# Performance work log

Measured on AMD Instinct MI355X. Metric: run time of the kernel, lower is better.

The kernel has to match this reference:

```python
import jax, jax.numpy as jnp
import numpy as np

NUM_HEAD = 16
MASKED_BIAS = -10000.0


def setup_inputs() -> dict:
    key = jax.random.key(0)
    k1, k2, k3 = jax.random.split(key, 3)
    B, M, N = 2, 2048, 1024
    x = jax.random.normal(k1, (B, M, N), dtype=jnp.float32)
    w_attn = jax.random.normal(k2, (N, 3 * N), dtype=jnp.float32) * 0.02
    w_proj = jax.random.normal(k3, (N, N), dtype=jnp.float32) * 0.02
    b_attn = jnp.zeros((3 * N,), dtype=jnp.float32)
    b_proj = jnp.zeros((N,), dtype=jnp.float32)
    return {"x": x, "w_attn": w_attn, "w_proj": w_proj,
            "b_attn": b_attn, "b_proj": b_proj}


def reference(x, w_attn, w_proj, b_attn, b_proj):
    B, M, N = x.shape
    H = NUM_HEAD
    d = N // H  # head dim
    # fused QKV projection: [B,M,3N]
    qkv = jnp.einsum('bmn,nd->bmd', x, w_attn) + b_attn
    q, k, v = jnp.split(qkv, 3, axis=-1)
    # split heads -> [B,H,M,d]
    q = q.reshape(B, M, H, d).transpose(0, 2, 1, 3)
    k = k.reshape(B, M, H, d).transpose(0, 2, 1, 3)
    v = v.reshape(B, M, H, d).transpose(0, 2, 1, 3)
    # scaled dot-product scores [B,H,M,M]
    scores = jnp.einsum('bhqd,bhkd->bhqk', q, k) / jnp.sqrt(jnp.float32(d))
    causal = jnp.tril(jnp.ones((M, M), dtype=bool))  # GPT-2 bias buffer
    scores = jnp.where(causal, scores, jnp.float32(MASKED_BIAS))
    attn = jax.nn.softmax(scores, axis=-1)
    # context [B,H,M,d] -> [B,M,N]
    ctx = jnp.einsum('bhqk,bhkd->bhqd', attn, v)
    ctx = ctx.transpose(0, 2, 1, 3).reshape(B, M, N)
    # output projection
    out = jnp.einsum('bmn,no->bmo', ctx, w_proj) + b_proj
    return out
```

## Files before the change

### kernel.cpp

```cpp
#include <hip/hip_runtime.h>

typedef __attribute__((ext_vector_type(8))) __bf16 bf16x8;
typedef __attribute__((ext_vector_type(4))) __bf16 bf16x4;
typedef __attribute__((ext_vector_type(4))) float f32x4;
typedef __attribute__((ext_vector_type(4))) short short4v;

__device__ __forceinline__ void async_copy16(const void* g, void* l) {
    __builtin_amdgcn_global_load_lds(
        (const __attribute__((address_space(1))) void*)g,
        (__attribute__((address_space(3))) void*)l, 16, 0, 0);
}

__global__ __launch_bounds__(256) void prep_k(
    const float* __restrict__ x, __bf16* __restrict__ xb,
    const float* __restrict__ wa, __bf16* __restrict__ wAt,
    const float* __restrict__ wp, __bf16* __restrict__ wPt)
{
    __shared__ float tile[32][33];
    const int bx = blockIdx.x;
    if (bx < 2048) {
        size_t i = ((size_t)bx * 256 + threadIdx.x) * 8;
        float4 a = *(const float4*)&x[i];
        float4 b = *(const float4*)&x[i + 4];
        bf16x8 o;
        o[0] = (__bf16)a.x; o[1] = (__bf16)a.y; o[2] = (__bf16)a.z; o[3] = (__bf16)a.w;
        o[4] = (__bf16)b.x; o[5] = (__bf16)b.y; o[6] = (__bf16)b.z; o[7] = (__bf16)b.w;
        *(bf16x8*)&xb[i] = o;
        return;
    }
    const float* src; __bf16* dst; int R, C, c0, r0;
    if (bx < 5120) {
        int id = bx - 2048;
        src = wa; dst = wAt; R = 1024; C = 3072;
        c0 = (id % 96) * 32; r0 = (id / 96) * 32;
    } else {
        int id = bx - 5120;
        src = wp; dst = wPt; R = 1024; C = 1024;
        c0 = (id & 31) * 32; r0 = (id >> 5) * 32;
    }
    int tx = threadIdx.x & 31, ty = threadIdx.x >> 5;
    for (int i = ty; i < 32; i += 8)
        tile[i][tx] = src[(size_t)(r0 + i) * C + (c0 + tx)];
    __syncthreads();
    for (int i = ty; i < 32; i += 8)
        dst[(size_t)(c0 + i) * R + (r0 + tx)] = (__bf16)tile[tx][i];
}

template <int MODE, int TN>
__global__ __launch_bounds__(256) void gemm_bt(
    const __bf16* __restrict__ A, const __bf16* __restrict__ Bt,
    const float* __restrict__ bias, int K,
    __bf16* __restrict__ O0, __bf16* __restrict__ O1, __bf16* __restrict__ O2,
    float* __restrict__ Of)
{
    constexpr int NJ = TN / 32;
    __shared__ __align__(16) __bf16 lds_a[2][128 * 32];
    __shared__ __align__(16) __bf16 lds_b[2][TN * 32];
    const int row0 = blockIdx.x * 128;
    const int col0 = blockIdx.y * TN;
    const int tid  = threadIdx.x;
    const int lane = tid & 63;
    const int w    = tid >> 6;
    const int wm   = (w >> 1) * 64, wn = (w & 1) * (TN / 2);
    const int quad = lane >> 4, l16 = lane & 15;

    auto stage = [&](int pb, int kb) {
#pragma unroll
        for (int t = 0; t < 2; ++t) {
            int s = t * 256 + tid;
            int L = s >> 3, c = (s & 7) ^ (L & 7);
            int row = 2 * L + (c >> 2), ch = c & 3;
            async_copy16(&A[(size_t)(row0 + row) * K + kb + ch * 8],
                         (char*)&lds_a[pb][0] + (t * 256 + w * 64) * 16);
        }
#pragma unroll
        for (int t = 0; t < TN / 64; ++t) {
            int s = t * 256 + tid;
            int L = s >> 3, c = (s & 7) ^ (L & 7);
            int row = 2 * L + (c >> 2), ch = c & 3;
            async_copy16(&Bt[(size_t)(col0 + row) * K + kb + ch * 8],
                         (char*)&lds_b[pb][0] + (t * 256 + w * 64) * 16);
        }
    };

    const int nIter = K >> 5;
    f32x4 acc[4][NJ] = {};
    stage(0, 0);
    for (int it = 0; it < nIter; ++it) {
        __syncthreads();
        if (it + 1 < nIter) stage((it + 1) & 1, (it + 1) << 5);
        const __bf16* la = &lds_a[it & 1][0];
        const __bf16* lb = &lds_b[it & 1][0];
        bf16x8 af[4], bfr[NJ];
#pragma unroll
        for (int i = 0; i < 4; ++i) {
            int r = wm + i * 16 + l16;
            int L = r >> 1, g = ((r & 1) * 4 + quad) ^ (L & 7);
            af[i] = *(const bf16x8*)&la[L * 64 + g * 8];
        }
#pragma unroll
        for (int j = 0; j < NJ; ++j) {
            int r = wn + j * 16 + l16;
            int L = r >> 1, g = ((r & 1) * 4 + quad) ^ (L & 7);
            bfr[j] = *(const bf16x8*)&lb[L * 64 + g * 8];
        }
#pragma unroll
        for (int i = 0; i < 4; ++i)
#pragma unroll
            for (int j = 0; j < NJ; ++j)
                acc[i][j] = __builtin_amdgcn_mfma_f32_16x16x32_bf16(
                    af[i], bfr[j], acc[i][j], 0, 0, 0);
    }

#pragma unroll
    for (int i = 0; i < 4; ++i) {
        int grow = row0 + wm + i * 16 + quad * 4;
#pragma unroll
        for (int j = 0; j < NJ; ++j) {
            int gcol = col0 + wn + j * 16 + l16;
            float bv = bias[gcol];
            if constexpr (MODE == 0) {
                int which = gcol >> 10;
                int n  = gcol & 1023;
                int hh = n >> 6, dd = n & 63;
                int bb = grow >> 11, mm0 = grow & 2047;
                int bhh = bb * 16 + hh;
                if (which == 2) {
                    int w64 = mm0 & 63;
                    int mi = (mm0 & ~63) | (w64 & 32) | ((w64 & 12) << 1)
                             | ((w64 & 16) >> 2);
                    bf16x4 pk;
#pragma unroll
                    for (int r = 0; r < 4; ++r)
                        pk[r] = (__bf16)(acc[i][j][r] + bv);
                    *(bf16x4*)&O2[((size_t)bhh * 64 + dd) * 2048 + mi] = pk;
                } else {
#pragma unroll
                    for (int r = 0; r < 4; ++r) {
                        float v = acc[i][j][r] + bv;
                        if (which == 0)
                            O0[((size_t)bhh * 2048 + mm0 + r) * 64 + dd] =
                                (__bf16)(v * 0.18033688011112042f);
                        else
                            O1[((size_t)bhh * 2048 + mm0 + r) * 64 + dd] =
                                (__bf16)v;
                    }
                }
            } else {
#pragma unroll
                for (int r = 0; r < 4; ++r) {
                    int gr = grow + r;
                    Of[(size_t)gr * 1024 + gcol] = acc[i][j][r] + bv;
                }
            }
        }
    }
}

__global__ __launch_bounds__(256) void attn_kernel(
    const __bf16* __restrict__ Qh, const __bf16* __restrict__ Kh,
    const __bf16* __restrict__ Vt, __bf16* __restrict__ ctx)
{
    const int M = 2048, D = 64;
    const int bh = blockIdx.x;
    const int qt = 31 - blockIdx.y;
    const int b = bh >> 4, h = bh & 15;
    const int tid = threadIdx.x, lane = tid & 63, w = tid >> 6;
    const int quad = lane >> 4, l16 = lane & 15;

    const int q0 = qt * 64;
    const int nIter = qt + 1;

    __shared__ __align__(16) __bf16 lds_k[2][64 * 64];
    __shared__ __align__(16) __bf16 lds_v[2][64 * 64];

    const __bf16* Qp = Qh + (size_t)bh * M * D;
    const __bf16* Kp = Kh + (size_t)bh * M * D;
    const __bf16* Vp = Vt + (size_t)bh * D * M;

    const int qw = q0 + w * 16;

    bf16x8 qf[2];
#pragma unroll
    for (int c = 0; c < 2; ++c)
        qf[c] = *(const bf16x8*)
            &Qp[(size_t)(qw + l16) * D + c * 32 + quad * 8];

    f32x4 acc2[4] = {};
    f32x4 acc_s = {};
    const short4v ones2 = {0x3F80, 0x3F80, 0x3F80, 0x3F80};

    auto stage = [&](int pb, int kb) {
#pragma unroll
        for (int t = 0; t < 2; ++t) {
            int c = w * 128 + t * 64 + lane;
            int row = c >> 3, ch = c & 7;
            int gch = ch ^ (row & 7);
            async_copy16(&Kp[(size_t)(kb + row) * 64 + gch * 8],
                         (char*)&lds_k[pb][0] + (w * 128 + t * 64) * 16);
            async_copy16(&Vp[(size_t)row * M + kb + gch * 8],
                         (char*)&lds_v[pb][0] + (w * 128 + t * 64) * 16);
        }
    };

    stage(0, 0);

    for (int it = 0; it < nIter; ++it) {
        const int kb = it << 6;
        __syncthreads();
        if (it + 1 < nIter) stage((it + 1) & 1, kb + 64);
        const __bf16* kt = &lds_k[it & 1][0];
        const __bf16* vt = &lds_v[it & 1][0];

        f32x4 s[4];
#pragma unroll
        for (int t = 0; t < 4; ++t) {
            f32x4 tt = {};
#pragma unroll
            for (int c = 0; c < 2; ++c) {
                int ch = ((c << 2) + quad) ^ (l16 & 7);
                bf16x8 kf = *(const bf16x8*)
                    &kt[(((t << 4) + l16) << 6) + (ch << 3)];
                tt = __builtin_amdgcn_mfma_f32_16x16x32_bf16(
                    kf, qf[c], tt, 0, 0, 0);
            }
            s[t] = tt;
        }
        if (kb + 63 > qw) {
#pragma unroll
            for (int t = 0; t < 4; ++t)
#pragma unroll
                for (int r = 0; r < 4; ++r)
                    if (kb + t * 16 + quad * 4 + r > qw + l16)
                        s[t][r] = -1e30f;
        }
        short4v pf[4];
#pragma unroll
        for (int t = 0; t < 4; ++t) {
            bf16x4 pk;
#pragma unroll
            for (int r = 0; r < 4; ++r)
                pk[r] = (__bf16)exp2f(s[t][r]);
            pf[t] = *(short4v*)&pk;
        }
#pragma unroll
        for (int f = 0; f < 4; ++f) {
            int row = (f << 4) + l16;
#pragma unroll
            for (int tp = 0; tp < 2; ++tp) {
                int g = ((tp << 2) + quad) ^ (row & 7);
                bf16x8 vv = *(const bf16x8*)&vt[(row << 6) + (g << 3)];
                bf16x4 lo = {vv[0], vv[1], vv[2], vv[3]};
                bf16x4 hi = {vv[4], vv[5], vv[6], vv[7]};
                acc2[f] = __builtin_amdgcn_mfma_f32_16x16x16bf16_1k(
                    *(short4v*)&lo, pf[2 * tp], acc2[f], 0, 0, 0);
                acc2[f] = __builtin_amdgcn_mfma_f32_16x16x16bf16_1k(
                    *(short4v*)&hi, pf[2 * tp + 1], acc2[f], 0, 0, 0);
            }
        }
#pragma unroll
        for (int t = 0; t < 4; ++t)
            acc_s = __builtin_amdgcn_mfma_f32_16x16x16bf16_1k(
                ones2, pf[t], acc_s, 0, 0, 0);
    }

    __syncthreads();
    __bf16* ldsT = &lds_k[0][0];
    const float l = acc_s[0];
#pragma unroll
    for (int f = 0; f < 4; ++f) {
        bf16x4 ov;
#pragma unroll
        for (int r = 0; r < 4; ++r)
            ov[r] = (__bf16)(acc2[f][r] / l);
        *(bf16x4*)&ldsT[(w * 16 + l16) * 72 + f * 16 + quad * 4] = ov;
    }
    __syncthreads();
    {
        int qq = tid >> 2;
        int dp = (tid & 3) * 16;
        const __bf16* src = &ldsT[qq * 72 + dp];
        __bf16* dst = &ctx[((size_t)(b * 2048 + q0 + qq)) * 1024 + h * 64 + dp];
        *(bf16x8*)&dst[0] = *(const bf16x8*)&src[0];
        *(bf16x8*)&dst[8] = *(const bf16x8*)&src[8];
    }
}

extern "C" void kernel_launch(void* const* d_in, const int* in_sizes, int n_in,
                              void* d_out, int out_size, void* d_ws, size_t ws_size,
                              hipStream_t stream) {
    const float* x      = (const float*)d_in[0];
    const float* w_attn = (const float*)d_in[1];
    const float* w_proj = (const float*)d_in[2];
    const float* b_attn = (const float*)d_in[3];
    const float* b_proj = (const float*)d_in[4];
    float* out = (float*)d_out;

    char* ws = (char*)d_ws;
    __bf16* xb  = (__bf16*)(ws);
    __bf16* ctx = (__bf16*)(ws);
    __bf16* wAt = (__bf16*)(ws + 8388608);
    __bf16* wPt = (__bf16*)(ws + 14680064);
    __bf16* Vt  = (__bf16*)(ws + 16777216);
    __bf16* Qh  = (__bf16*)d_out;
    __bf16* Kh  = (__bf16*)d_out + 4194304;

    prep_k<<<6144, 256, 0, stream>>>(x, xb, w_attn, wAt, w_proj, wPt);
    gemm_bt<0, 128><<<dim3(32, 24), 256, 0, stream>>>(xb, wAt, b_attn, 1024,
                                                      Qh, Kh, Vt, nullptr);
    attn_kernel<<<dim3(32, 32), 256, 0, stream>>>(Qh, Kh, Vt, ctx);
    gemm_bt<1, 64><<<dim3(32, 16), 256, 0, stream>>>(ctx, wPt, b_proj, 1024,
                                                     nullptr, nullptr, nullptr, out);
}
```

Baseline: 177.6 us.

## Split long causal attention tiles across two blocks and combine partial sums

The 16 longest query tiles per head are each split into two key-range halves run by separate blocks. Each half writes an unnormalized numerator and its row sums, and a new combine kernel adds the halves and normalizes. The goal is to even out the triangular causal workload and shorten the tail of the attention grid. The change also adds an early skip for fully masked key blocks per wave and replaces pairs of 16x16x16 MFMAs with single 16x16x32 MFMAs. Costs are an extra kernel launch, extra global traffic for the partials, and an extra bf16 rounding of the unnormalized partial numerators.

```diff
diff --git a/kernel.cpp b/kernel.cpp
--- a/kernel.cpp
+++ b/kernel.cpp
@@ -3,7 +3,6 @@
 typedef __attribute__((ext_vector_type(8))) __bf16 bf16x8;
 typedef __attribute__((ext_vector_type(4))) __bf16 bf16x4;
 typedef __attribute__((ext_vector_type(4))) float f32x4;
-typedef __attribute__((ext_vector_type(4))) short short4v;
 
 __device__ __forceinline__ void async_copy16(const void* g, void* l) {
     __builtin_amdgcn_global_load_lds(
@@ -159,17 +158,29 @@
 
 __global__ __launch_bounds__(256) void attn_kernel(
     const __bf16* __restrict__ Qh, const __bf16* __restrict__ Kh,
-    const __bf16* __restrict__ Vt, __bf16* __restrict__ ctx)
+    const __bf16* __restrict__ Vt, __bf16* __restrict__ ctx,
+    __bf16* __restrict__ pnum, float* __restrict__ lbuf)
 {
     const int M = 2048, D = 64;
     const int bh = blockIdx.x;
-    const int qt = 31 - blockIdx.y;
+    const int y = blockIdx.y;
     const int b = bh >> 4, h = bh & 15;
     const int tid = threadIdx.x, lane = tid & 63, w = tid >> 6;
     const int quad = lane >> 4, l16 = lane & 15;
 
+    int qt, part, t0, t1;
+    bool split;
+    if (y < 32) {
+        qt = 31 - (y >> 1); part = y & 1; split = true;
+        int half = (qt + 1) >> 1;
+        t0 = part ? half : 0;
+        t1 = part ? (qt + 1) : half;
+    } else {
+        qt = 47 - y; part = 0; split = false;
+        t0 = 0; t1 = qt + 1;
+    }
     const int q0 = qt * 64;
-    const int nIter = qt + 1;
+    const int nIter = t1 - t0;
 
     __shared__ __align__(16) __bf16 lds_k[2][64 * 64];
     __shared__ __align__(16) __bf16 lds_v[2][64 * 64];
@@ -188,7 +199,8 @@
 
     f32x4 acc2[4] = {};
     f32x4 acc_s = {};
-    const short4v ones2 = {0x3F80, 0x3F80, 0x3F80, 0x3F80};
+    const __bf16 onev = (__bf16)1.0f;
+    const bf16x8 ones8 = {onev, onev, onev, onev, onev, onev, onev, onev};
 
     auto stage = [&](int pb, int kb) {
 #pragma unroll
@@ -203,14 +215,15 @@
         }
     };
 
-    stage(0, 0);
-
-    for (int it = 0; it < nIter; ++it) {
-        const int kb = it << 6;
+    stage(0, t0 << 6);
+
+    for (int i = 0; i < nIter; ++i) {
+        const int kb = (t0 + i) << 6;
         __syncthreads();
-        if (it + 1 < nIter) stage((it + 1) & 1, kb + 64);
-        const __bf16* kt = &lds_k[it & 1][0];
-        const __bf16* vt = &lds_v[it & 1][0];
+        if (i + 1 < nIter) stage((i + 1) & 1, kb + 64);
+        if (kb > qw + 15) continue;
+        const __bf16* kt = &lds_k[i & 1][0];
+        const __bf16* vt = &lds_v[i & 1][0];
 
         f32x4 s[4];
 #pragma unroll
@@ -234,14 +247,16 @@
                     if (kb + t * 16 + quad * 4 + r > qw + l16)
                         s[t][r] = -1e30f;
         }
-        short4v pf[4];
-#pragma unroll
-        for (int t = 0; t < 4; ++t) {
-            bf16x4 pk;
-#pragma unroll
-            for (int r = 0; r < 4; ++r)
-                pk[r] = (__bf16)exp2f(s[t][r]);
-            pf[t] = *(short4v*)&pk;
+        bf16x8 pf32[2];
+#pragma unroll
+        for (int tp = 0; tp < 2; ++tp) {
+            bf16x8 pp;
+#pragma unroll
+            for (int r = 0; r < 4; ++r) {
+                pp[r]     = (__bf16)exp2f(s[2 * tp][r]);
+                pp[4 + r] = (__bf16)exp2f(s[2 * tp + 1][r]);
+            }
+            pf32[tp] = pp;
         }
 #pragma unroll
         for (int f = 0; f < 4; ++f) {
@@ -250,29 +265,30 @@
             for (int tp = 0; tp < 2; ++tp) {
                 int g = ((tp << 2) + quad) ^ (row & 7);
                 bf16x8 vv = *(const bf16x8*)&vt[(row << 6) + (g << 3)];
-                bf16x4 lo = {vv[0], vv[1], vv[2], vv[3]};
-                bf16x4 hi = {vv[4], vv[5], vv[6], vv[7]};
-                acc2[f] = __builtin_amdgcn_mfma_f32_16x16x16bf16_1k(
-                    *(short4v*)&lo, pf[2 * tp], acc2[f], 0, 0, 0);
-                acc2[f] = __builtin_amdgcn_mfma_f32_16x16x16bf16_1k(
-                    *(short4v*)&hi, pf[2 * tp + 1], acc2[f], 0, 0, 0);
+                acc2[f] = __builtin_amdgcn_mfma_f32_16x16x32_bf16(
+                    vv, pf32[tp], acc2[f], 0, 0, 0);
             }
         }
 #pragma unroll
-        for (int t = 0; t < 4; ++t)
-            acc_s = __builtin_amdgcn_mfma_f32_16x16x16bf16_1k(
-                ones2, pf[t], acc_s, 0, 0, 0);
+        for (int tp = 0; tp < 2; ++tp)
+            acc_s = __builtin_amdgcn_mfma_f32_16x16x32_bf16(
+                ones8, pf32[tp], acc_s, 0, 0, 0);
     }
 
     __syncthreads();
     __bf16* ldsT = &lds_k[0][0];
     const float l = acc_s[0];
+    const int tileIdx = bh * 16 + (qt - 16);
+    if (split && quad == 0)
+        lbuf[tileIdx * 128 + part * 64 + w * 16 + l16] = l;
 #pragma unroll
     for (int f = 0; f < 4; ++f) {
         bf16x4 ov;
 #pragma unroll
-        for (int r = 0; r < 4; ++r)
-            ov[r] = (__bf16)(acc2[f][r] / l);
+        for (int r = 0; r < 4; ++r) {
+            float v = acc2[f][r];
+            ov[r] = (__bf16)(split ? v : v / l);
+        }
         *(bf16x4*)&ldsT[(w * 16 + l16) * 72 + f * 16 + quad * 4] = ov;
     }
     __syncthreads();
@@ -280,10 +296,43 @@
         int qq = tid >> 2;
         int dp = (tid & 3) * 16;
         const __bf16* src = &ldsT[qq * 72 + dp];
-        __bf16* dst = &ctx[((size_t)(b * 2048 + q0 + qq)) * 1024 + h * 64 + dp];
+        __bf16* dst;
+        if (split && part == 1)
+            dst = &pnum[(size_t)tileIdx * 4096 + qq * 64 + dp];
+        else
+            dst = &ctx[((size_t)(b * 2048 + q0 + qq)) * 1024 + h * 64 + dp];
         *(bf16x8*)&dst[0] = *(const bf16x8*)&src[0];
         *(bf16x8*)&dst[8] = *(const bf16x8*)&src[8];
     }
+}
+
+__global__ __launch_bounds__(256) void combine_k(
+    __bf16* __restrict__ ctx, const __bf16* __restrict__ pnum,
+    const float* __restrict__ lbuf)
+{
+    const int bh = blockIdx.x, t = blockIdx.y;
+    const int b = bh >> 4, h = bh & 15;
+    const int tileIdx = bh * 16 + t;
+    const int q0 = (16 + t) * 64;
+    const int tid = threadIdx.x;
+    const int qq = tid >> 2, dp = (tid & 3) * 16;
+
+    float la = lbuf[tileIdx * 128 + qq];
+    float lb = lbuf[tileIdx * 128 + 64 + qq];
+    float inv = 1.0f / (la + lb);
+
+    __bf16* crow = &ctx[((size_t)(b * 2048 + q0 + qq)) * 1024 + h * 64 + dp];
+    const __bf16* prow = &pnum[(size_t)tileIdx * 4096 + qq * 64 + dp];
+    bf16x8 a0 = *(const bf16x8*)&crow[0], a1 = *(const bf16x8*)&crow[8];
+    bf16x8 b0 = *(const bf16x8*)&prow[0], b1 = *(const bf16x8*)&prow[8];
+    bf16x8 o0, o1;
+#pragma unroll
+    for (int e = 0; e < 8; ++e) {
+        o0[e] = (__bf16)(((float)a0[e] + (float)b0[e]) * inv);
+        o1[e] = (__bf16)(((float)a1[e] + (float)b1[e]) * inv);
+    }
+    *(bf16x8*)&crow[0] = o0;
+    *(bf16x8*)&crow[8] = o1;
 }
 
 extern "C" void kernel_launch(void* const* d_in, const int* in_sizes, int n_in,
@@ -297,18 +346,21 @@
     float* out = (float*)d_out;
 
     char* ws = (char*)d_ws;
-    __bf16* xb  = (__bf16*)(ws);
-    __bf16* ctx = (__bf16*)(ws);
-    __bf16* wAt = (__bf16*)(ws + 8388608);
-    __bf16* wPt = (__bf16*)(ws + 14680064);
-    __bf16* Vt  = (__bf16*)(ws + 16777216);
-    __bf16* Qh  = (__bf16*)d_out;
-    __bf16* Kh  = (__bf16*)d_out + 4194304;
+    __bf16* xb   = (__bf16*)(ws);
+    __bf16* ctx  = (__bf16*)(ws);
+    __bf16* wAt  = (__bf16*)(ws + 8388608);
+    __bf16* pnum = (__bf16*)(ws + 8388608);
+    float*  lbuf = (float*)(ws + 12582912);
+    __bf16* wPt  = (__bf16*)(ws + 14680064);
+    __bf16* Vt   = (__bf16*)(ws + 16777216);
+    __bf16* Qh   = (__bf16*)d_out;
+    __bf16* Kh   = (__bf16*)d_out + 4194304;
 
     prep_k<<<6144, 256, 0, stream>>>(x, xb, w_attn, wAt, w_proj, wPt);
     gemm_bt<0, 128><<<dim3(32, 24), 256, 0, stream>>>(xb, wAt, b_attn, 1024,
                                                       Qh, Kh, Vt, nullptr);
-    attn_kernel<<<dim3(32, 32), 256, 0, stream>>>(Qh, Kh, Vt, ctx);
+    attn_kernel<<<dim3(32, 48), 256, 0, stream>>>(Qh, Kh, Vt, ctx, pnum, lbuf);
+    combine_k<<<dim3(32, 16), 256, 0, stream>>>(ctx, pnum, lbuf);
     gemm_bt<1, 64><<<dim3(32, 16), 256, 0, stream>>>(ctx, wPt, b_proj, 1024,
                                                      nullptr, nullptr, nullptr, out);
 }
```

Measured after the change: 180.0 us. No clear change (+1.4%).
